# Kernel tuning notes

Hardware: AMD Instinct MI355X
Metric: run time of the kernel (lower is better)

The kernel has to match this reference:

```python
import jax, jax.numpy as jnp
import numpy as np


def setup_inputs() -> dict:
    key = jax.random.key(0)
    k1, k2, k3, k4, k5 = jax.random.split(key, 5)
    B, IN_N, POSE = 32, 8192, 64
    M = 8                     # matrix_pose_dim = sqrt(64)
    NH, S2, HID = 32, 256, 256  # in_n/(img^2), img^2, hidden_dim
    OUT_N = 64
    return {
        "current_pose": jax.random.normal(k1, (B, IN_N, POSE), jnp.float32),
        "w_current": 0.02 * jax.random.normal(k2, (1, 1, IN_N, M, M), jnp.float32),
        "w_next": 0.02 * jax.random.normal(k3, (OUT_N, M, M), jnp.float32),
        "E_proj": 0.02 * jax.random.normal(k4, (NH, S2, HID), jnp.float32),
        "rel_embedd": jax.random.normal(k5, (1, 1, POSE), jnp.float32),
    }


def reference(current_pose, w_current, w_next, E_proj, rel_embedd):
    B, IN_N, POSE = current_pose.shape
    M = w_current.shape[-1]           # matrix_pose_dim
    NH, S2, HID = E_proj.shape        # heads, img*img, hidden_dim
    OUT_N = w_next.shape[0]

    # w_current: (1,1,IN_N,M,M) -> (1,IN_N,M,M); per-capsule pose-matrix multiply
    wc = w_current.reshape(IN_N, M, M)[None]
    cp = current_pose.reshape(B, IN_N, M, M)
    cp = jnp.matmul(cp, wc)                      # (B, IN_N, M, M)

    # raw reshape (row-major, matches torch .reshape) then Linformer projection
    cp = cp.reshape(B, POSE, NH, 1, S2)
    cp = jnp.matmul(cp, E_proj)                  # (B, POSE, NH, 1, HID)
    cp = cp[:, :, :, 0, :]                       # squeeze(3) -> (B, POSE, NH, HID)
    cp = cp.reshape(B, NH * HID, POSE)           # raw reshape as in torch

    # dots = softmax over out_n axis of a constant tensor == uniform 1/OUT_N.
    # einsum('bij,bje->bie') with uniform dots == mean over j, broadcast over i.
    pooled = jnp.sum(cp, axis=1, keepdims=True) / OUT_N   # (B, 1, POSE)
    npc = jnp.broadcast_to(pooled, (B, OUT_N, POSE))

    # add relative embedding (h_out = w_out = output_img_size = 1)
    npc = npc.reshape(B, OUT_N, 1, 1, POSE) + rel_embedd  # (B,OUT_N,1,1,POSE)
    npc = jnp.transpose(npc, (0, 2, 3, 1, 4)).reshape(B, OUT_N, POSE)

    # next-layer pose-matrix multiply
    npc = npc.reshape(B, OUT_N, M, M)
    npc = jnp.matmul(npc, w_next[None])           # (B, OUT_N, M, M)
    npc = npc.reshape(B, 1, 1, OUT_N, POSE)
    return npc[:, 0]                              # squeeze(1) -> (B,1,OUT_N,POSE)
```

## Files before the change

kernel.cpp:

```cpp
#include <hip/hip_runtime.h>
#include <hip/hip_bf16.h>


typedef short short8_t __attribute__((ext_vector_type(8)));
typedef float f32x4_t __attribute__((ext_vector_type(4)));
typedef int   int4_t  __attribute__((ext_vector_type(4)));

__device__ __forceinline__ short f2bf(float f) {
    union { float f; unsigned u; } v; v.f = f;
    unsigned r = v.u + 0x7FFFu + ((v.u >> 16) & 1u);
    return (short)(r >> 16);
}

__device__ __forceinline__ int cvt_pk(float x, float y) {
    int r;
    asm("v_cvt_pk_bf16_f32 %0, %1, %2" : "=v"(r) : "v"(x), "v"(y));
    return r;
}

__global__ void k_prep(const float* __restrict__ WC, short* __restrict__ WCf,
                       const float* __restrict__ E, float* __restrict__ F) {
    if (blockIdx.x < 256) {
        int t   = blockIdx.x * 256 + threadIdx.x;
        int l   = t & 63;
        int pc  = (t >> 6) & 15;
        int rp  = t >> 10;
        int lhi = l >> 4;
        int j   = l & 15;
        int row = (pc * 4 + lhi) * 128 + rp * 2 + (j >> 3);
        const float* src = WC + ((size_t)row << 6) + (j & 7);
        short8_t o;
        #pragma unroll
        for (int k = 0; k < 8; ++k) o[k] = f2bf(src[k * 8]);
        ((short8_t*)WCf)[t] = o;
    } else {
        int idx = ((blockIdx.x - 256) * 256 + threadIdx.x) * 4;
        int q   = idx & 63;
        int row = idx >> 6;
        int r   = row >> 6;
        int e   = row & 63;
        int nh  = r >> 2;
        int s2  = ((r & 3) << 6) + e;
        const float* base = E + (((size_t)nh * 256 + s2) << 8) + q;
        float4 s0 = *(const float4*)(base);
        float4 s1 = *(const float4*)(base + 64);
        float4 s2v = *(const float4*)(base + 128);
        float4 s3 = *(const float4*)(base + 192);
        float4 o;
        o.x = s0.x + s1.x + s2v.x + s3.x;
        o.y = s0.y + s1.y + s2v.y + s3.y;
        o.z = s0.z + s1.z + s2v.z + s3.z;
        o.w = s0.w + s1.w + s2v.w + s3.w;
        *(float4*)(F + idx) = o;
    }
}

__global__ void __launch_bounds__(512)
k_bc(const float* __restrict__ CP, const short* __restrict__ WCf,
     const float* __restrict__ F, float* __restrict__ P) {
    int gx   = blockIdx.x;
    int half = gx & 1;
    int rpg  = gx >> 1;
    int b0   = blockIdx.y * 2;
    int w = threadIdx.x >> 6;
    int l = threadIdx.x & 63;
    int b_loc  = w & 1;
    int rp_loc = w >> 1;
    int rp = rpg * 4 + rp_loc;
    int r0 = rp * 2;
    int b  = b0 + b_loc;

    int i16   = l & 15;
    int r_sel = i16 >> 3;
    int m1    = i16 & 7;
    int lhi   = l >> 4;

    __shared__ float Stile[2][512];

    const float* cp_base = CP + ((size_t)b << 19) + ((size_t)(r0 + r_sel) << 6) + m1 * 8;
    const short8_t* wf   = (const short8_t*)WCf + (size_t)rp * 1024 + (half * 8) * 64 + l;

    f32x4_t acc = {0.f, 0.f, 0.f, 0.f};
    #pragma unroll
    for (int c = 0; c < 8; ++c) {
        int p = (half * 8 + c) * 4 + lhi;
        const float* a_ptr = cp_base + ((size_t)p << 13);
        float4 a0 = *(const float4*)(a_ptr);
        float4 a1 = *(const float4*)(a_ptr + 4);
        int4_t ai;
        ai[0] = cvt_pk(a0.x, a0.y);
        ai[1] = cvt_pk(a0.z, a0.w);
        ai[2] = cvt_pk(a1.x, a1.y);
        ai[3] = cvt_pk(a1.z, a1.w);
        acc = __builtin_amdgcn_mfma_f32_16x16x32_bf16(
            __builtin_bit_cast(short8_t, ai), wf[c * 64], acc, 0, 0, 0);
    }
    int col = i16;
    #pragma unroll
    for (int v = 0; v < 4; ++v) {
        int row = lhi * 4 + v;
        if (row < 8 && col < 8)
            Stile[b_loc][rp_loc * 128 + row * 8 + col] = acc[v];
        else if (row >= 8 && col >= 8)
            Stile[b_loc][rp_loc * 128 + 64 + (row - 8) * 8 + (col - 8)] = acc[v];
    }
    __syncthreads();

    int g  = l >> 4;
    int ql = l & 15;
    const float* Fb = F + (((size_t)rpg * 512 + w * 64 + g) << 6) + ql * 4;
    f32x4_t p0 = {0.f, 0.f, 0.f, 0.f};
    f32x4_t p1 = {0.f, 0.f, 0.f, 0.f};
    #pragma unroll 4
    for (int s = 0; s < 16; ++s) {
        int jl = w * 64 + s * 4 + g;
        float4 fv = *(const float4*)(Fb + ((size_t)(s * 4) << 6));
        float s0 = Stile[0][jl];
        float s1 = Stile[1][jl];
        p0[0] += s0 * fv.x; p0[1] += s0 * fv.y; p0[2] += s0 * fv.z; p0[3] += s0 * fv.w;
        p1[0] += s1 * fv.x; p1[1] += s1 * fv.y; p1[2] += s1 * fv.z; p1[3] += s1 * fv.w;
    }
    #pragma unroll
    for (int c = 0; c < 4; ++c) {
        p0[c] += __shfl_xor(p0[c], 16, 64);
        p0[c] += __shfl_xor(p0[c], 32, 64);
        p1[c] += __shfl_xor(p1[c], 16, 64);
        p1[c] += __shfl_xor(p1[c], 32, 64);
    }
    if (l < 16) {
        int sp = (rpg * 2 + half) * 8 + w;
        float4 o0; o0.x = p0[0]; o0.y = p0[1]; o0.z = p0[2]; o0.w = p0[3];
        float4 o1; o1.x = p1[0]; o1.y = p1[1]; o1.z = p1[2]; o1.w = p1[3];
        *(float4*)(P + ((size_t)((b0 + 0) * 256 + sp) << 6) + ql * 4) = o0;
        *(float4*)(P + ((size_t)((b0 + 1) * 256 + sp) << 6) + ql * 4) = o1;
    }
}

__global__ void k_final(const float* __restrict__ P, const float* __restrict__ rel,
                        const float* __restrict__ WN, float* __restrict__ out) {
    int b  = blockIdx.x;
    int t  = threadIdx.x;
    int q    = t & 63;
    int sgrp = t >> 6;
    const float* Pb = P + ((size_t)b << 14);
    float s = 0.f;
    #pragma unroll 8
    for (int c = sgrp * 64; c < sgrp * 64 + 64; ++c)
        s += Pb[((size_t)c << 6) + q];
    __shared__ float red[4][64];
    red[sgrp][q] = s;
    __syncthreads();
    __shared__ float pool_s[64];
    if (t < 64) {
        pool_s[t] = (red[0][t] + red[1][t] + red[2][t] + red[3][t]) * (1.0f / 64.0f)
                    + rel[t];
    }
    __syncthreads();
    #pragma unroll
    for (int idx = t; idx < 4096; idx += 256) {
        int o = idx >> 6;
        int e = idx & 63;
        int m1 = e >> 3, m2 = e & 7;
        float a = 0.f;
        #pragma unroll
        for (int k = 0; k < 8; ++k)
            a += pool_s[m1 * 8 + k] * WN[o * 64 + k * 8 + m2];
        out[((size_t)b << 12) + idx] = a;
    }
}

extern "C" void kernel_launch(void* const* d_in, const int* in_sizes, int n_in,
                              void* d_out, int out_size, void* d_ws, size_t ws_size,
                              hipStream_t stream) {
    const float* current_pose = (const float*)d_in[0];
    const float* w_current    = (const float*)d_in[1];
    const float* w_next       = (const float*)d_in[2];
    const float* E_proj       = (const float*)d_in[3];
    const float* rel_embedd   = (const float*)d_in[4];
    float* out = (float*)d_out;

    char* ws = (char*)d_ws;
    float* F   = (float*)(ws);
    short* WCf = (short*)(ws + (2u << 20));
    float* P   = (float*)(ws + (3u << 20));

    k_prep<<<dim3(768), dim3(256), 0, stream>>>(w_current, WCf, E_proj, F);
    k_bc<<<dim3(32, 16), dim3(512), 0, stream>>>(current_pose, WCf, F, P);
    k_final<<<dim3(32), dim3(256), 0, stream>>>(P, rel_embedd, w_next, out);
}
```

Baseline: 29.70 us.

## Reduce partials in-block, split MFMA accumulator chain, shrink partial buffer

Each k_bc block now sums its eight waves' partial vectors in shared memory and writes one 64-float row per batch, instead of eight rows. This cuts the partial buffer P and k_final's read loop from 256 rows per batch to 32. The MFMA loop also uses two independent accumulators to shorten the dependency chain and issue loads earlier, and launch bounds request 4 waves per EU occupancy. The cost is an extra __syncthreads and a small shared-memory reduction, plus a changed floating-point summation order.

```diff
diff --git a/kernel.cpp b/kernel.cpp
--- a/kernel.cpp
+++ b/kernel.cpp
@@ -55,7 +55,7 @@
     }
 }
 
-__global__ void __launch_bounds__(512)
+__global__ void __launch_bounds__(512, 4)
 k_bc(const float* __restrict__ CP, const short* __restrict__ WCf,
      const float* __restrict__ F, float* __restrict__ P) {
     int gx   = blockIdx.x;
@@ -76,25 +76,43 @@
     int lhi   = l >> 4;
 
     __shared__ float Stile[2][512];
+    __shared__ float redp[8][2][64];
 
     const float* cp_base = CP + ((size_t)b << 19) + ((size_t)(r0 + r_sel) << 6) + m1 * 8;
     const short8_t* wf   = (const short8_t*)WCf + (size_t)rp * 1024 + (half * 8) * 64 + l;
 
-    f32x4_t acc = {0.f, 0.f, 0.f, 0.f};
-    #pragma unroll
-    for (int c = 0; c < 8; ++c) {
-        int p = (half * 8 + c) * 4 + lhi;
-        const float* a_ptr = cp_base + ((size_t)p << 13);
-        float4 a0 = *(const float4*)(a_ptr);
-        float4 a1 = *(const float4*)(a_ptr + 4);
-        int4_t ai;
-        ai[0] = cvt_pk(a0.x, a0.y);
-        ai[1] = cvt_pk(a0.z, a0.w);
-        ai[2] = cvt_pk(a1.x, a1.y);
-        ai[3] = cvt_pk(a1.z, a1.w);
-        acc = __builtin_amdgcn_mfma_f32_16x16x32_bf16(
-            __builtin_bit_cast(short8_t, ai), wf[c * 64], acc, 0, 0, 0);
-    }
+    f32x4_t acc0 = {0.f, 0.f, 0.f, 0.f};
+    f32x4_t acc1 = {0.f, 0.f, 0.f, 0.f};
+    #pragma unroll
+    for (int cc = 0; cc < 4; ++cc) {
+        int pA = (half * 8 + cc) * 4 + lhi;
+        int pB = (half * 8 + cc + 4) * 4 + lhi;
+        const float* aA = cp_base + ((size_t)pA << 13);
+        const float* aB = cp_base + ((size_t)pB << 13);
+        float4 a0 = *(const float4*)(aA);
+        float4 a1 = *(const float4*)(aA + 4);
+        float4 c0 = *(const float4*)(aB);
+        float4 c1 = *(const float4*)(aB + 4);
+        short8_t wfA = wf[cc * 64];
+        short8_t wfB = wf[(cc + 4) * 64];
+        int4_t aiA, aiB;
+        aiA[0] = cvt_pk(a0.x, a0.y);
+        aiA[1] = cvt_pk(a0.z, a0.w);
+        aiA[2] = cvt_pk(a1.x, a1.y);
+        aiA[3] = cvt_pk(a1.z, a1.w);
+        aiB[0] = cvt_pk(c0.x, c0.y);
+        aiB[1] = cvt_pk(c0.z, c0.w);
+        aiB[2] = cvt_pk(c1.x, c1.y);
+        aiB[3] = cvt_pk(c1.z, c1.w);
+        acc0 = __builtin_amdgcn_mfma_f32_16x16x32_bf16(
+            __builtin_bit_cast(short8_t, aiA), wfA, acc0, 0, 0, 0);
+        acc1 = __builtin_amdgcn_mfma_f32_16x16x32_bf16(
+            __builtin_bit_cast(short8_t, aiB), wfB, acc1, 0, 0, 0);
+    }
+    f32x4_t acc;
+    #pragma unroll
+    for (int v = 0; v < 4; ++v) acc[v] = acc0[v] + acc1[v];
+
     int col = i16;
     #pragma unroll
     for (int v = 0; v < 4; ++v) {
@@ -108,7 +126,7 @@
 
     int g  = l >> 4;
     int ql = l & 15;
-    const float* Fb = F + (((size_t)rpg * 512 + w * 64 + g) << 6) + ql * 4;
+    const float* Fb = F + (((size_t)(rpg * 512 + w * 64 + g)) << 6) + ql * 4;
     f32x4_t p0 = {0.f, 0.f, 0.f, 0.f};
     f32x4_t p1 = {0.f, 0.f, 0.f, 0.f};
     #pragma unroll 4
@@ -128,11 +146,18 @@
         p1[c] += __shfl_xor(p1[c], 32, 64);
     }
     if (l < 16) {
-        int sp = (rpg * 2 + half) * 8 + w;
-        float4 o0; o0.x = p0[0]; o0.y = p0[1]; o0.z = p0[2]; o0.w = p0[3];
-        float4 o1; o1.x = p1[0]; o1.y = p1[1]; o1.z = p1[2]; o1.w = p1[3];
-        *(float4*)(P + ((size_t)((b0 + 0) * 256 + sp) << 6) + ql * 4) = o0;
-        *(float4*)(P + ((size_t)((b0 + 1) * 256 + sp) << 6) + ql * 4) = o1;
+        *(f32x4_t*)(&redp[w][0][ql * 4]) = p0;
+        *(f32x4_t*)(&redp[w][1][ql * 4]) = p1;
+    }
+    __syncthreads();
+
+    if (threadIdx.x < 128) {
+        int bb = threadIdx.x >> 6;
+        int q  = threadIdx.x & 63;
+        float s = 0.f;
+        #pragma unroll
+        for (int ww = 0; ww < 8; ++ww) s += redp[ww][bb][q];
+        P[((size_t)((b0 + bb) * 32 + gx) << 6) + q] = s;
     }
 }
 
@@ -142,10 +167,10 @@
     int t  = threadIdx.x;
     int q    = t & 63;
     int sgrp = t >> 6;
-    const float* Pb = P + ((size_t)b << 14);
+    const float* Pb = P + ((size_t)(b * 32) << 6);
     float s = 0.f;
-    #pragma unroll 8
-    for (int c = sgrp * 64; c < sgrp * 64 + 64; ++c)
+    #pragma unroll
+    for (int c = sgrp * 8; c < sgrp * 8 + 8; ++c)
         s += Pb[((size_t)c << 6) + q];
     __shared__ float red[4][64];
     red[sgrp][q] = s;
```

Result: no change. 30.12 us (+1.4%).
